# Performance work log

Measured on AMD Instinct MI355X. Metric: run time of the kernel, lower is better.

## Reference

```python
import jax, jax.numpy as jnp
import numpy as np

N_NODES = 50000
N_EDGES = 800000
GEN_EPS = 1e-7
LN_EPS = 1e-5


def _mlp3_tanh(x, w0, b0, w1, b1, w2, b2):
    x = jnp.tanh(x @ w0.T + b0)
    x = jnp.tanh(x @ w1.T + b1)
    return jnp.tanh(x @ w2.T + b2)


def _gen_conv(x, src, dst, edge_attr, w0, b0, ln_w, ln_b, w1, b1):
    # GENConv(aggr='softmax', t=1): msg = relu(x_j + e) + eps
    msg = jax.nn.relu(x[src] + edge_attr) + GEN_EPS          # [E, 64]
    m = jax.ops.segment_max(msg, dst, num_segments=N_NODES)  # [N, 64]
    ex = jnp.exp(msg - m[dst])
    den = jax.ops.segment_sum(ex, dst, num_segments=N_NODES)
    alpha = ex / den[dst]                                    # scatter-softmax per dst
    agg = jax.ops.segment_sum(alpha * msg, dst, num_segments=N_NODES)
    h = x + agg                                              # x_r + aggregated messages
    # internal MLP: Linear(64->128), LayerNorm(128), ReLU, Linear(128->64)
    h = h @ w0.T + b0
    mu = jnp.mean(h, axis=-1, keepdims=True)
    var = jnp.mean((h - mu) ** 2, axis=-1, keepdims=True)
    h = ln_w * (h - mu) * jax.lax.rsqrt(var + LN_EPS) + ln_b
    h = jax.nn.relu(h)
    return h @ w1.T + b1


def setup_inputs() -> dict:
    key = jax.random.key(0)
    ks = jax.random.split(key, 32)
    s = 0.05
    d = {
        'node_features': jax.random.normal(ks[0], (N_NODES, 11), jnp.float32),
        'edge_features': jax.random.normal(ks[1], (N_EDGES, 3), jnp.float32),
        'edge_index': jax.random.randint(ks[2], (2, N_EDGES), 0, N_NODES, jnp.int32),
        'ne_w0': jax.random.normal(ks[3], (64, 11)) * s, 'ne_b0': jnp.zeros((64,)),
        'ne_w1': jax.random.normal(ks[4], (64, 64)) * s, 'ne_b1': jnp.zeros((64,)),
        'ne_w2': jax.random.normal(ks[5], (64, 64)) * s, 'ne_b2': jnp.zeros((64,)),
        'ee_w0': jax.random.normal(ks[6], (64, 3)) * s, 'ee_b0': jnp.zeros((64,)),
        'ee_w1': jax.random.normal(ks[7], (64, 64)) * s, 'ee_b1': jnp.zeros((64,)),
        'ee_w2': jax.random.normal(ks[8], (64, 64)) * s, 'ee_b2': jnp.zeros((64,)),
        'mp_w0': jax.random.normal(ks[9], (3, 128, 64)) * s,
        'mp_b0': jnp.zeros((3, 128)),
        'mp_ln_w': jnp.ones((3, 128)), 'mp_ln_b': jnp.zeros((3, 128)),
        'mp_w1': jax.random.normal(ks[10], (3, 64, 128)) * s,
        'mp_b1': jnp.zeros((3, 64)),
        'pi_w0': jax.random.normal(ks[11], (64, 64)) * s, 'pi_b0': jnp.zeros((64,)),
        'pi_w1': jax.random.normal(ks[12], (64, 64)) * s, 'pi_b1': jnp.zeros((64,)),
        'pi_w2': jax.random.normal(ks[13], (2, 64)) * s, 'pi_b2': jnp.zeros((2,)),
    }
    return {k: (v.astype(jnp.float32) if v.dtype != jnp.int32 else v) for k, v in d.items()}


def reference(node_features, edge_features, edge_index,
              ne_w0, ne_b0, ne_w1, ne_b1, ne_w2, ne_b2,
              ee_w0, ee_b0, ee_w1, ee_b1, ee_w2, ee_b2,
              mp_w0, mp_b0, mp_ln_w, mp_ln_b, mp_w1, mp_b1,
              pi_w0, pi_b0, pi_w1, pi_b1, pi_w2, pi_b2):
    src, dst = edge_index[0], edge_index[1]
    x = _mlp3_tanh(node_features, ne_w0, ne_b0, ne_w1, ne_b1, ne_w2, ne_b2)
    e = _mlp3_tanh(edge_features, ee_w0, ee_b0, ee_w1, ee_b1, ee_w2, ee_b2)
    for i in range(3):
        x = _gen_conv(x, src, dst, e, mp_w0[i], mp_b0[i], mp_ln_w[i], mp_ln_b[i], mp_w1[i], mp_b1[i])
    h = jnp.tanh(x @ pi_w0.T + pi_b0)
    h = jnp.tanh(h @ pi_w1.T + pi_b1)
    out = h @ pi_w2.T + pi_b2                 # [N, 2]
    # output.t().reshape(-1)[:n_turbines] == first column of out
    means = -30.0 + (out[:, 0] + 1.0) * 60.0 / 2.0
    return means
```

## Files before the change

### kernel.cpp

```cpp
#include <hip/hip_runtime.h>
#include <hip/hip_fp16.h>
#include <stdint.h>

#define N_NODES 50000
#define N_EDGES 800000

typedef unsigned short u16;
typedef unsigned int u32;
typedef __attribute__((ext_vector_type(8))) short short8;
typedef __attribute__((ext_vector_type(4))) float f32x4;
typedef __attribute__((ext_vector_type(4))) u32 u32x4;
typedef __attribute__((ext_vector_type(2))) u32 u32x2;

#define WAVE_SYNC() asm volatile("s_waitcnt lgkmcnt(0)" ::: "memory")

__device__ __forceinline__ float b2f(u16 v) {
    u32 u = ((u32)v) << 16; float f; __builtin_memcpy(&f, &u, 4); return f;
}
__device__ __forceinline__ u16 f2b(float f) {
    u32 u; __builtin_memcpy(&u, &f, 4);
    return (u16)((u + 0x8000u) >> 16);
}
__device__ __forceinline__ float lo2f(u32 p) {
    u32 u = p << 16; float f; __builtin_memcpy(&f, &u, 4); return f;
}
__device__ __forceinline__ float hi2f(u32 p) {
    u32 u = p & 0xffff0000u; float f; __builtin_memcpy(&f, &u, 4); return f;
}
__device__ __forceinline__ u32 pack2(float a, float b) {
    u32 ua, ub; __builtin_memcpy(&ua, &a, 4); __builtin_memcpy(&ub, &b, 4);
    return __builtin_amdgcn_perm(ub + 0x8000u, ua + 0x8000u, 0x07060302u);
}
__device__ __forceinline__ f32x4 mfma16(short8 a, short8 b, f32x4 c) {
    return __builtin_amdgcn_mfma_f32_16x16x32_bf16(a, b, c, 0, 0, 0);
}

__device__ __forceinline__ bool detect_bf(const void* nf) {
    u32 w = ((const u32*)nf)[threadIdx.x & 63];
    u32 lo = w & 0xffffu;
    int e = (int)((lo >> 7) & 0xff);
    int good = ((e >= 118 && e <= 132) || lo == 0) ? 1 : 0;
    unsigned long long b = __ballot(good != 0);
    return __popcll(b) >= 48;
}

#define TANH_TBL_N 256
__device__ __forceinline__ void load_tbl(const u32* __restrict__ g, u32* tbl) {
    int i = (int)threadIdx.x;
    if (i < TANH_TBL_N) tbl[i] = g[i];
    __syncthreads();
}
__device__ __forceinline__ float lut_tanh(const u32* __restrict__ tbl, float x) {
    float a = __builtin_fabsf(x);
    a = fminf(a, 7.96875f);
    int i = (int)(a * 32.f);
    u32 e = tbl[i];
    __half2 h2; __builtin_memcpy(&h2, &e, 4);
    float b = __half2float(__low2half(h2));
    float s = __half2float(__high2half(h2));
    return copysignf(fmaf(s, a, b), x);
}

enum : int {
    NE_B0 = 704,   NE_B1 = 4864,  NE_B2 = 9024,
    EE_B0 = 9280,  EE_B1 = 13440, EE_B2 = 17600,
    MP_B0 = 42240, LNW_O = 42624, LNB_O = 43008, MP_B1 = 67968,
    PI_B0 = 72256, PI_B1 = 76416, PI_W2 = 76480, PI_B2 = 76608,
    W_TOTAL = 76610
};

enum : int {
    FR_EE1 = 0, FR_EE2 = 4, FR_EE3 = 12, FR_NE1 = 20, FR_NE2 = 24, FR_NE3 = 32,
    FR_MP0 = 40, FR_MP1 = 88, FR_PI0 = 136, FR_PI1 = 144, FR_TOTAL = 152
};

#define OFF_W       ((size_t)0)
#define OFF_WB      ((size_t)0x61000)
#define OFF_TBL     ((size_t)0x88000)
#define OFF_XB0     ((size_t)0x90000)
#define OFF_XB1     ((size_t)0x700000)
#define OFF_H64B    ((size_t)0xE00000)
#define OFF_E       ((size_t)0x1500000)
#define OFF_ROWPTR  ((size_t)0x8300000)
#define OFF_CURSOR  ((size_t)0x8340000)
#define OFF_CNT     ((size_t)0x8380000)
#define OFF_PERM    ((size_t)0x83C0000)
#define OFF_SRCS    ((size_t)0x8700000)
#define OFF_BSUM    ((size_t)0x8A80000)

struct Ptrs24 { const void* p[24]; };

__global__ void prep_kernel(const void* nf, Ptrs24 ps, float* __restrict__ W,
                            u16* __restrict__ Wb, u32* __restrict__ gtbl) {
    bool bf = detect_bf(nf);
    int t = blockIdx.x * blockDim.x + threadIdx.x;
    if (t < FR_TOTAL * 512) {
        const int base[15] = {FR_EE1,FR_EE2,FR_EE3,FR_NE1,FR_NE2,FR_NE3,
                              FR_MP0,FR_MP0+16,FR_MP0+32, FR_MP1,FR_MP1+16,FR_MP1+32,
                              FR_PI0,FR_PI1,FR_TOTAL};
        const int psrc[14]  = {6,8,10, 0,2,4, 12,12,12, 16,16,16, 18,20};
        const int soff[14]  = {0,0,0, 0,0,0, 0,8192,16384, 0,8192,16384, 0,0};
        const int kreal[14] = {3,64,64, 11,64,64, 64,64,64, 128,128,128, 64,64};
        const int nn[14]    = {64,64,64, 64,64,64, 128,128,128, 64,64,64, 64,64};
        int f = t >> 9, r = t & 511, lane = r >> 3, j = r & 7;
        int l = 0;
        while (f >= base[l + 1]) l++;
        int lf = f - base[l];
        int NT = nn[l] >> 4;
        int kt = lf / NT, nt = lf % NT;
        int k = kt * 32 + (lane >> 4) * 8 + j;
        int n = nt * 16 + (lane & 15);
        float v = 0.f;
        if (k < kreal[l]) {
            long idx = (long)soff[l] + (long)n * kreal[l] + k;
            const void* p = ps.p[psrc[l]];
            v = bf ? b2f(((const u16*)p)[idx]) : ((const float*)p)[idx];
        }
        u32 u; __builtin_memcpy(&u, &v, 4);
        Wb[t] = (u16)((u + 0x7fffu + ((u >> 16) & 1u)) >> 16);
        return;
    }
    int t2 = t - FR_TOTAL * 512;
    if (t2 < 1986) {
        const int cnt[14]  = {64,64,64, 64,64,64, 384,384,384,192, 64,64,128,2};
        const int wdst[14] = {NE_B0,NE_B1,NE_B2, EE_B0,EE_B1,EE_B2,
                              MP_B0,LNW_O,LNB_O,MP_B1, PI_B0,PI_B1,PI_W2,PI_B2};
        const int sp[14]   = {1,3,5, 7,9,11, 13,14,15,17, 19,21,22,23};
        int sgi = 0, off = t2;
        while (off >= cnt[sgi]) { off -= cnt[sgi]; sgi++; }
        const void* p = ps.p[sp[sgi]];
        W[wdst[sgi] + off] = bf ? b2f(((const u16*)p)[off]) : ((const float*)p)[off];
        return;
    }
    int i = t2 - 1986;
    if (i < TANH_TBL_N) {
        float x0 = i * 0.03125f, x1 = x0 + 0.03125f;
        float t0 = tanhf(x0), t1 = tanhf(x1);
        float s = (t1 - t0) * 32.f;
        float b = fmaf(-s, x0, t0);
        __half hs = __float2half(s), hb = __float2half(b);
        u16 us, ub;
        __builtin_memcpy(&us, &hs, 2); __builtin_memcpy(&ub, &hb, 2);
        gtbl[i] = (u32)ub | ((u32)us << 16);
    }
}


__global__ void hist_kernel(const int* __restrict__ dst, int* __restrict__ cnts) {
    int e = blockIdx.x * blockDim.x + threadIdx.x;
    if (e < N_EDGES) atomicAdd(&cnts[dst[e]], 1);
}

__global__ void scanA(const int* __restrict__ cnts, int* __restrict__ prow,
                      int* __restrict__ bsum) {
    __shared__ int wsum[16];
    int tid = threadIdx.x, lane = tid & 63, wid = tid >> 6;
    int i0 = blockIdx.x * 2048 + tid * 2;
    int v0 = 0, v1 = 0;
    if (i0 >= 1 && i0 <= N_NODES) v0 = (cnts[i0 - 1] + 1) & ~1;
    if (i0 + 1 <= N_NODES && i0 + 1 >= 1) v1 = (cnts[i0] + 1) & ~1;
    int v = v0 + v1;
#pragma unroll
    for (int off = 1; off < 64; off <<= 1) {
        int t = __shfl_up(v, off, 64);
        if (lane >= off) v += t;
    }
    if (lane == 63) wsum[wid] = v;
    __syncthreads();
    if (tid == 0) { int a = 0; for (int w = 0; w < 16; w++) { a += wsum[w]; wsum[w] = a; } }
    __syncthreads();
    int incl = v + (wid ? wsum[wid - 1] : 0);
    if (i0 <= N_NODES) prow[i0] = incl - v1;
    if (i0 + 1 <= N_NODES) prow[i0 + 1] = incl;
    if (tid == 1023) bsum[blockIdx.x] = incl;
}
__global__ void scanC(const int* __restrict__ bsum, const int* __restrict__ cnts,
                      int* __restrict__ prow, int* __restrict__ cursor,
                      int* __restrict__ srcs) {
    int i = blockIdx.x * 1024 + threadIdx.x;
    if (i > N_NODES) return;
    int nb = (int)(blockIdx.x >> 1);
    int add = 0;
    for (int b = 0; b < nb; b++) add += bsum[b];
    int v = prow[i] + add;
    prow[i] = v;
    if (i < N_NODES) {
        cursor[i] = v;
        int c = cnts[i];
        if (c & 1) srcs[v + c] = -1;
    }
}

__global__ void scatter_kernel(const int* __restrict__ dst, const int* __restrict__ src,
                               int* __restrict__ cursor, int* __restrict__ perm,
                               int* __restrict__ srcs) {
    int e = blockIdx.x * blockDim.x + threadIdx.x;
    if (e >= N_EDGES) return;
    int p = atomicAdd(&cursor[dst[e]], 1);
    perm[e] = p;
    srcs[p] = src[e];
}


template<int KT, int NT, int INSTR>
__device__ __forceinline__ void mfma_layer(const u32* ldsin, int lane,
        const short8* __restrict__ Wf, int basef, const float* __restrict__ bias, f32x4* acc) {
    int q = lane >> 4, mr = lane & 15;
#pragma unroll
    for (int nt = 0; nt < NT; nt++) acc[nt] = *(const f32x4*)(bias + nt * 16 + q * 4);
#pragma unroll
    for (int kt = 0; kt < KT; kt++) {
        short8 act = *(const short8*)(ldsin + mr * INSTR + kt * 16 + q * 4);
#pragma unroll
        for (int nt = 0; nt < NT; nt++)
            acc[nt] = mfma16(Wf[(basef + kt * NT + nt) * 64 + lane], act, acc[nt]);
    }
}

template<int KT, int NT>
__device__ __forceinline__ void mfma_layer_reg(const short8* act, int lane,
        const short8* __restrict__ Wf, int basef, const float* __restrict__ bias, f32x4* acc) {
    int q = lane >> 4;
#pragma unroll
    for (int nt = 0; nt < NT; nt++) acc[nt] = *(const f32x4*)(bias + nt * 16 + q * 4);
#pragma unroll
    for (int kt = 0; kt < KT; kt++)
#pragma unroll
        for (int nt = 0; nt < NT; nt++)
            acc[nt] = mfma16(Wf[(basef + kt * NT + nt) * 64 + lane], act[kt], acc[nt]);
}

template<int NT, int OUTSTR>
__device__ __forceinline__ void tanh_pack_lds(const f32x4* acc, u32* ldsout, int lane,
                                              const u32* __restrict__ tbl) {
    int q = lane >> 4, mr = lane & 15;
#pragma unroll
    for (int nt = 0; nt < NT; nt++) {
        f32x4 a = acc[nt];
        ldsout[mr * OUTSTR + nt * 8 + q * 2 + 0] = pack2(lut_tanh(tbl, a[0]), lut_tanh(tbl, a[1]));
        ldsout[mr * OUTSTR + nt * 8 + q * 2 + 1] = pack2(lut_tanh(tbl, a[2]), lut_tanh(tbl, a[3]));
    }
}

__device__ __forceinline__ void zero_stage(u32* B0, int lane) {
#pragma unroll
    for (int it = 0; it < 4; it++) {
        int f = lane + 64 * it;
        B0[(f >> 4) * 36 + (f & 15)] = 0;
    }
}


__global__ __launch_bounds__(256) void edge_encoder(const void* nf, const void* ef,
        u32* __restrict__ ebuf, const int* __restrict__ perm, const float* __restrict__ W,
        const short8* __restrict__ Wf, const u32* __restrict__ gtbl) {
    __shared__ u32 lds[4 * 1152];
    __shared__ u32 tbl[TANH_TBL_N];
    bool bf = detect_bf(nf);
    load_tbl(gtbl, tbl);
    int wv = threadIdx.x >> 6, lane = threadIdx.x & 63;
    u32* B0 = lds + wv * 1152;
    u32* B1 = B0 + 576;
    long ebase = (long)blockIdx.x * 64 + wv * 16;
    zero_stage(B0, lane);
    if (lane < 16) {
        long e = ebase + lane;
        float i0, i1, i2;
        if (bf) { const u16* p = (const u16*)ef + e * 3; i0 = b2f(p[0]); i1 = b2f(p[1]); i2 = b2f(p[2]); }
        else    { const float* p = (const float*)ef + e * 3; i0 = p[0]; i1 = p[1]; i2 = p[2]; }
        u32* row = B0 + lane * 36;
        row[0] = pack2(i0, i1); row[1] = pack2(i2, 0.f);
    }
    WAVE_SYNC();
    f32x4 acc[4];
    mfma_layer<1, 4, 36>(B0, lane, Wf, FR_EE1, W + EE_B0, acc);
    tanh_pack_lds<4, 36>(acc, B1, lane, tbl);
    WAVE_SYNC();
    mfma_layer<2, 4, 36>(B1, lane, Wf, FR_EE2, W + EE_B1, acc);
    tanh_pack_lds<4, 36>(acc, B0, lane, tbl);
    WAVE_SYNC();
    mfma_layer<2, 4, 36>(B0, lane, Wf, FR_EE3, W + EE_B2, acc);
    tanh_pack_lds<4, 36>(acc, B1, lane, tbl);
    WAVE_SYNC();
    int ro = lane >> 2, cc = (lane & 3) * 8;
    long e = ebase + ro;
    long prowp = perm[e];
    u32x4 v0 = *(const u32x4*)&B1[ro * 36 + cc];
    u32x4 v1 = *(const u32x4*)&B1[ro * 36 + cc + 4];
    *(u32x4*)&ebuf[prowp * 32 + cc] = v0;
    *(u32x4*)&ebuf[prowp * 32 + cc + 4] = v1;
}

__global__ __launch_bounds__(256) void node_encoder(const void* nf,
        u16* __restrict__ xbf, const float* __restrict__ W,
        const short8* __restrict__ Wf, const u32* __restrict__ gtbl) {
    __shared__ u32 lds[4 * 1152];
    __shared__ u32 tbl[TANH_TBL_N];
    bool bf = detect_bf(nf);
    load_tbl(gtbl, tbl);
    int wv = threadIdx.x >> 6, lane = threadIdx.x & 63;
    int q = lane >> 4, mr = lane & 15;
    u32* B0 = lds + wv * 1152;
    u32* B1 = B0 + 576;
    long nbase = (long)blockIdx.x * 64 + wv * 16;
    zero_stage(B0, lane);
    if (lane < 16) {
        long n = nbase + lane;
        if (n < N_NODES) {
            float in[11];
#pragma unroll
            for (int j = 0; j < 11; j++)
                in[j] = bf ? b2f(((const u16*)nf)[n * 11 + j]) : ((const float*)nf)[n * 11 + j];
            u32* row = B0 + lane * 36;
#pragma unroll
            for (int d = 0; d < 5; d++) row[d] = pack2(in[2 * d], in[2 * d + 1]);
            row[5] = pack2(in[10], 0.f);
        }
    }
    WAVE_SYNC();
    f32x4 acc[4];
    mfma_layer<1, 4, 36>(B0, lane, Wf, FR_NE1, W + NE_B0, acc);
    tanh_pack_lds<4, 36>(acc, B1, lane, tbl);
    WAVE_SYNC();
    mfma_layer<2, 4, 36>(B1, lane, Wf, FR_NE2, W + NE_B1, acc);
    tanh_pack_lds<4, 36>(acc, B0, lane, tbl);
    WAVE_SYNC();
    mfma_layer<2, 4, 36>(B0, lane, Wf, FR_NE3, W + NE_B2, acc);
    long n = nbase + mr;
    if (n < N_NODES) {
#pragma unroll
        for (int nt = 0; nt < 4; nt++) {
            float v0 = lut_tanh(tbl, acc[nt][0]), v1 = lut_tanh(tbl, acc[nt][1]);
            float v2 = lut_tanh(tbl, acc[nt][2]), v3 = lut_tanh(tbl, acc[nt][3]);
            u32x2 pb; pb.x = pack2(v0, v1); pb.y = pack2(v2, v3);
            *(u32x2*)&xbf[n * 64 + nt * 16 + q * 4] = pb;
        }
    }
}

template<int R>
__global__ __launch_bounds__(256) void aggregate_kernel(
        const u32* __restrict__ xbf32, const u32* __restrict__ ebuf32,
        const int* __restrict__ srcs, const int* __restrict__ prow,
        u32* __restrict__ h64bf32) {
    __shared__ int ldsW[4][64];
    int wv = threadIdx.x >> 6;
    int wid = (int)((blockIdx.x * 256 + threadIdx.x) >> 6);
    int lane = (int)(threadIdx.x & 63);
    int n0 = __builtin_amdgcn_readfirstlane(wid) * 2;
    if (n0 >= N_NODES) return;
    int half = lane >> 5, h = lane & 31;
    int rl = n0 + (lane < 2 ? lane : 2);
    int rv = prow[rl];
    int kb0 = __shfl(rv, 0, 64);
    int kb1 = __shfl(rv, 1, 64);
    int kb2 = __shfl(rv, 2, 64);
    float num[2][2], den[2][2];
#pragma unroll
    for (int j = 0; j < 2; j++) { num[j][0] = num[j][1] = den[j][0] = den[j][1] = 0.f; }
    for (int wb = kb0; wb < kb2; wb += 64) {
        ldsW[wv][lane] = srcs[wb + lane];
        WAVE_SYNC();
        int we = wb + 64;
        int hi0 = kb1 < we ? kb1 : we;
        int lo1 = kb1 > wb ? kb1 : wb;
        int hi1 = kb2 < we ? kb2 : we;
#pragma unroll 4
        for (int k = wb; k < hi0; k += 2) {
            int s = ldsW[wv][k - wb + half];
            u32 ev = ebuf32[(size_t)(k + half) * 32 + h];
            u32 xv = xbf32[(size_t)(s > 0 ? s : 0) * 32 + h];
            float m0 = fmaxf(lo2f(xv) + lo2f(ev), 0.f) + 1e-7f;
            float m1 = fmaxf(hi2f(xv) + hi2f(ev), 0.f) + 1e-7f;
            float w0 = __expf(m0), w1 = __expf(m1);
            if (s < 0) { w0 = 0.f; w1 = 0.f; }
            num[0][0] = fmaf(w0, m0, num[0][0]); den[0][0] += w0;
            num[0][1] = fmaf(w1, m1, num[0][1]); den[0][1] += w1;
        }
#pragma unroll 4
        for (int k = lo1; k < hi1; k += 2) {
            int s = ldsW[wv][k - wb + half];
            u32 ev = ebuf32[(size_t)(k + half) * 32 + h];
            u32 xv = xbf32[(size_t)(s > 0 ? s : 0) * 32 + h];
            float m0 = fmaxf(lo2f(xv) + lo2f(ev), 0.f) + 1e-7f;
            float m1 = fmaxf(hi2f(xv) + hi2f(ev), 0.f) + 1e-7f;
            float w0 = __expf(m0), w1 = __expf(m1);
            if (s < 0) { w0 = 0.f; w1 = 0.f; }
            num[1][0] = fmaf(w0, m0, num[1][0]); den[1][0] += w0;
            num[1][1] = fmaf(w1, m1, num[1][1]); den[1][1] += w1;
        }
        WAVE_SYNC();
    }
#pragma unroll
    for (int j = 0; j < 2; j++) {
        float n0f = num[j][0] + __shfl_xor(num[j][0], 32, 64);
        float d0f = den[j][0] + __shfl_xor(den[j][0], 32, 64);
        float n1f = num[j][1] + __shfl_xor(num[j][1], 32, 64);
        float d1f = den[j][1] + __shfl_xor(den[j][1], 32, 64);
        if (half == 0) {
            float agg0 = (d0f > 0.f) ? __fdividef(n0f, d0f) : 0.f;
            float agg1 = (d1f > 0.f) ? __fdividef(n1f, d1f) : 0.f;
            u32 xr = xbf32[(size_t)(n0 + j) * 32 + h];
            h64bf32[(size_t)(n0 + j) * 32 + h] = pack2(lo2f(xr) + agg0, hi2f(xr) + agg1);
        }
    }
}

__global__ __launch_bounds__(256) void mlp_fused(const u16* __restrict__ h64bf,
        u16* __restrict__ xbf,
        const float* __restrict__ W, const short8* __restrict__ Wf, int r) {
    __shared__ u32 lds[4 * 1088];
    int wv = threadIdx.x >> 6, lane = threadIdx.x & 63;
    int q = lane >> 4, mr = lane & 15;
    u32* bufY = lds + wv * 1088;
    long nbase = (long)blockIdx.x * 64 + wv * 16;
    long row = nbase + mr;
    long rc = (row < N_NODES) ? row : (N_NODES - 1);
    short8 act[2];
#pragma unroll
    for (int kt = 0; kt < 2; kt++)
        act[kt] = *(const short8*)&h64bf[rc * 64 + kt * 32 + q * 8];
    f32x4 acc[8];
    mfma_layer_reg<2, 8>(act, lane, Wf, FR_MP0 + r * 16, W + MP_B0 + r * 128, acc);
    float s = 0.f, sq = 0.f;
#pragma unroll
    for (int nt = 0; nt < 8; nt++)
#pragma unroll
        for (int rr = 0; rr < 4; rr++) { float v = acc[nt][rr]; s += v; sq = fmaf(v, v, sq); }
    s += __shfl_xor(s, 16, 64);  s += __shfl_xor(s, 32, 64);
    sq += __shfl_xor(sq, 16, 64); sq += __shfl_xor(sq, 32, 64);
    float mu = s * (1.f / 128.f);
    float var = sq * (1.f / 128.f) - mu * mu;
    float inv = rsqrtf(var + 1e-5f);
    const float* LW = W + LNW_O + r * 128;
    const float* LB = W + LNB_O + r * 128;
#pragma unroll
    for (int nt = 0; nt < 8; nt++) {
        f32x4 lw = *(const f32x4*)(LW + nt * 16 + q * 4);
        f32x4 lb = *(const f32x4*)(LB + nt * 16 + q * 4);
        float u0 = fmaxf(fmaf((acc[nt][0] - mu) * inv, lw[0], lb[0]), 0.f);
        float u1 = fmaxf(fmaf((acc[nt][1] - mu) * inv, lw[1], lb[1]), 0.f);
        float u2 = fmaxf(fmaf((acc[nt][2] - mu) * inv, lw[2], lb[2]), 0.f);
        float u3 = fmaxf(fmaf((acc[nt][3] - mu) * inv, lw[3], lb[3]), 0.f);
        bufY[mr * 68 + nt * 8 + q * 2 + 0] = pack2(u0, u1);
        bufY[mr * 68 + nt * 8 + q * 2 + 1] = pack2(u2, u3);
    }
    WAVE_SYNC();
    f32x4 acc2[4];
    mfma_layer<4, 4, 68>(bufY, lane, Wf, FR_MP1 + r * 16, W + MP_B1 + r * 64, acc2);
    if (row < N_NODES) {
#pragma unroll
        for (int nt = 0; nt < 4; nt++) {
            f32x4 v = acc2[nt];
            u32x2 pb; pb.x = pack2(v[0], v[1]); pb.y = pack2(v[2], v[3]);
            *(u32x2*)&xbf[row * 64 + nt * 16 + q * 4] = pb;
        }
    }
}

__global__ __launch_bounds__(256) void policy_head(const void* nf,
        const u16* __restrict__ xbf, void* out, const float* __restrict__ W,
        const short8* __restrict__ Wf, const u32* __restrict__ gtbl) {
    __shared__ u32 lds[4 * 576];
    __shared__ u32 tbl[TANH_TBL_N];
    bool bf = detect_bf(nf);
    load_tbl(gtbl, tbl);
    int wv = threadIdx.x >> 6, lane = threadIdx.x & 63;
    int q = lane >> 4, mr = lane & 15;
    u32* bufY = lds + wv * 576;
    long nbase = (long)blockIdx.x * 64 + wv * 16;
    long row = nbase + mr;
    long rc = (row < N_NODES) ? row : (N_NODES - 1);
    short8 act[2];
#pragma unroll
    for (int kt = 0; kt < 2; kt++)
        act[kt] = *(const short8*)&xbf[rc * 64 + kt * 32 + q * 8];
    f32x4 acc[4];
    mfma_layer_reg<2, 4>(act, lane, Wf, FR_PI0, W + PI_B0, acc);
    tanh_pack_lds<4, 36>(acc, bufY, lane, tbl);
    WAVE_SYNC();
    mfma_layer<2, 4, 36>(bufY, lane, Wf, FR_PI1, W + PI_B1, acc);
    float o = 0.f;
#pragma unroll
    for (int nt = 0; nt < 4; nt++) {
        f32x4 w2 = *(const f32x4*)(W + PI_W2 + nt * 16 + q * 4);
#pragma unroll
        for (int rr = 0; rr < 4; rr++) o = fmaf(lut_tanh(tbl, acc[nt][rr]), w2[rr], o);
    }
    o += __shfl_xor(o, 16, 64);
    o += __shfl_xor(o, 32, 64);
    if (lane < 16 && row < N_NODES) {
        float means = 30.f * (o + W[PI_B2]);
        if (bf) ((u16*)out)[row] = f2b(means);
        else    ((float*)out)[row] = means;
    }
}

extern "C" void kernel_launch(void* const* d_in, const int* in_sizes, int n_in,
                              void* d_out, int out_size, void* d_ws, size_t ws_size,
                              hipStream_t stream) {
    char* ws = (char*)d_ws;
    float* W      = (float*)(ws + OFF_W);
    u16*   Wb     = (u16*)(ws + OFF_WB);
    const short8* Wf = (const short8*)(ws + OFF_WB);
    u32*   gtbl   = (u32*)(ws + OFF_TBL);
    u16*   xb0    = (u16*)(ws + OFF_XB0);
    u16*   xb1    = (u16*)(ws + OFF_XB1);
    u16*   h64bf  = (u16*)(ws + OFF_H64B);
    u32*   h64b32 = (u32*)(ws + OFF_H64B);
    u32*   ebuf32 = (u32*)(ws + OFF_E);
    int*   prow   = (int*)(ws + OFF_ROWPTR);
    int*   cursor = (int*)(ws + OFF_CURSOR);
    int*   cnts   = (int*)(ws + OFF_CNT);
    int*   perm   = (int*)(ws + OFF_PERM);
    int*   srcs   = (int*)(ws + OFF_SRCS);
    int*   bsum   = (int*)(ws + OFF_BSUM);

    const void* nf  = d_in[0];
    const int* ei   = (const int*)d_in[2];
    const int* srcv = ei;
    const int* dstv = ei + N_EDGES;

    hipMemsetAsync(cnts, 0, N_NODES * sizeof(int), stream);

    Ptrs24 ps;
    for (int k = 0; k < 24; k++) ps.p[k] = d_in[3 + k];
    prep_kernel<<<(FR_TOTAL * 512 + 1986 + TANH_TBL_N + 255) / 256, 256, 0, stream>>>(
        nf, ps, W, Wb, gtbl);

    hist_kernel<<<(N_EDGES + 255) / 256, 256, 0, stream>>>(dstv, cnts);
    scanA<<<25, 1024, 0, stream>>>(cnts, prow, bsum);
    scanC<<<(N_NODES + 1024) / 1024, 1024, 0, stream>>>(bsum, cnts, prow, cursor, srcs);
    scatter_kernel<<<(N_EDGES + 255) / 256, 256, 0, stream>>>(dstv, srcv, cursor, perm, srcs);

    node_encoder<<<(N_NODES + 63) / 64, 256, 0, stream>>>(nf, xb0, W, Wf, gtbl);
    edge_encoder<<<N_EDGES / 64, 256, 0, stream>>>(nf, d_in[1], ebuf32, perm, W, Wf, gtbl);

    u16* xbc = xb0; u16* xbn = xb1;
    const int aggBlocks = (N_NODES / 2 * 64) / 256;
    aggregate_kernel<0><<<aggBlocks, 256, 0, stream>>>((const u32*)xbc, ebuf32, srcs, prow, h64b32);
    mlp_fused<<<(N_NODES + 63) / 64, 256, 0, stream>>>(h64bf, xbn, W, Wf, 0);
    { u16* tb = xbc; xbc = xbn; xbn = tb; }
    aggregate_kernel<1><<<aggBlocks, 256, 0, stream>>>((const u32*)xbc, ebuf32, srcs, prow, h64b32);
    mlp_fused<<<(N_NODES + 63) / 64, 256, 0, stream>>>(h64bf, xbn, W, Wf, 1);
    { u16* tb = xbc; xbc = xbn; xbn = tb; }
    aggregate_kernel<2><<<aggBlocks, 256, 0, stream>>>((const u32*)xbc, ebuf32, srcs, prow, h64b32);
    mlp_fused<<<(N_NODES + 63) / 64, 256, 0, stream>>>(h64bf, xbn, W, Wf, 2);
    { u16* tb = xbc; xbc = xbn; xbn = tb; }

    policy_head<<<(N_NODES + 63) / 64, 256, 0, stream>>>(nf, xbc, d_out, W, Wf, gtbl);
}
```

Before: 420.8 us.

## Fold count zeroing into prep, widen aggregation loads, write edge encodings directly

Zeroing of the histogram counts moves into prep_kernel, so the separate memset launch goes away. The edge encoder writes its final tanh output straight to the permuted global edge buffer instead of staging it through LDS. LDS stores in the tanh/LayerNorm paths are merged into 64-bit writes. The aggregation kernel now handles four edges per iteration, with each lane loading 8-byte pairs instead of 4-byte words. This raises memory-level parallelism but adds tail masking and uses smaller, 8-byte scattered global writes in the edge encoder.

```diff
diff --git a/kernel.cpp b/kernel.cpp
--- a/kernel.cpp
+++ b/kernel.cpp
@@ -90,11 +90,17 @@
 
 struct Ptrs24 { const void* p[24]; };
 
+#define PREP_FRAG   (FR_TOTAL * 512)
+#define PREP_BIAS   (PREP_FRAG + 1986)
+#define PREP_LUT    (PREP_BIAS + TANH_TBL_N)
+#define PREP_TOTAL  (PREP_LUT + N_NODES)
+
 __global__ void prep_kernel(const void* nf, Ptrs24 ps, float* __restrict__ W,
-                            u16* __restrict__ Wb, u32* __restrict__ gtbl) {
+                            u16* __restrict__ Wb, u32* __restrict__ gtbl,
+                            int* __restrict__ cnts) {
     bool bf = detect_bf(nf);
     int t = blockIdx.x * blockDim.x + threadIdx.x;
-    if (t < FR_TOTAL * 512) {
+    if (t < PREP_FRAG) {
         const int base[15] = {FR_EE1,FR_EE2,FR_EE3,FR_NE1,FR_NE2,FR_NE3,
                               FR_MP0,FR_MP0+16,FR_MP0+32, FR_MP1,FR_MP1+16,FR_MP1+32,
                               FR_PI0,FR_PI1,FR_TOTAL};
@@ -120,8 +126,8 @@
         Wb[t] = (u16)((u + 0x7fffu + ((u >> 16) & 1u)) >> 16);
         return;
     }
-    int t2 = t - FR_TOTAL * 512;
-    if (t2 < 1986) {
+    if (t < PREP_BIAS) {
+        int t2 = t - PREP_FRAG;
         const int cnt[14]  = {64,64,64, 64,64,64, 384,384,384,192, 64,64,128,2};
         const int wdst[14] = {NE_B0,NE_B1,NE_B2, EE_B0,EE_B1,EE_B2,
                               MP_B0,LNW_O,LNB_O,MP_B1, PI_B0,PI_B1,PI_W2,PI_B2};
@@ -132,8 +138,8 @@
         W[wdst[sgi] + off] = bf ? b2f(((const u16*)p)[off]) : ((const float*)p)[off];
         return;
     }
-    int i = t2 - 1986;
-    if (i < TANH_TBL_N) {
+    if (t < PREP_LUT) {
+        int i = t - PREP_BIAS;
         float x0 = i * 0.03125f, x1 = x0 + 0.03125f;
         float t0 = tanhf(x0), t1 = tanhf(x1);
         float s = (t1 - t0) * 32.f;
@@ -142,7 +148,9 @@
         u16 us, ub;
         __builtin_memcpy(&us, &hs, 2); __builtin_memcpy(&ub, &hb, 2);
         gtbl[i] = (u32)ub | ((u32)us << 16);
-    }
+        return;
+    }
+    if (t < PREP_TOTAL) cnts[t - PREP_LUT] = 0;
 }
 
 
@@ -237,8 +245,10 @@
 #pragma unroll
     for (int nt = 0; nt < NT; nt++) {
         f32x4 a = acc[nt];
-        ldsout[mr * OUTSTR + nt * 8 + q * 2 + 0] = pack2(lut_tanh(tbl, a[0]), lut_tanh(tbl, a[1]));
-        ldsout[mr * OUTSTR + nt * 8 + q * 2 + 1] = pack2(lut_tanh(tbl, a[2]), lut_tanh(tbl, a[3]));
+        u32x2 pb;
+        pb.x = pack2(lut_tanh(tbl, a[0]), lut_tanh(tbl, a[1]));
+        pb.y = pack2(lut_tanh(tbl, a[2]), lut_tanh(tbl, a[3]));
+        *(u32x2*)&ldsout[mr * OUTSTR + nt * 8 + q * 2] = pb;
     }
 }
 
@@ -259,6 +269,7 @@
     bool bf = detect_bf(nf);
     load_tbl(gtbl, tbl);
     int wv = threadIdx.x >> 6, lane = threadIdx.x & 63;
+    int q = lane >> 4, mr = lane & 15;
     u32* B0 = lds + wv * 1152;
     u32* B1 = B0 + 576;
     long ebase = (long)blockIdx.x * 64 + wv * 16;
@@ -280,15 +291,15 @@
     tanh_pack_lds<4, 36>(acc, B0, lane, tbl);
     WAVE_SYNC();
     mfma_layer<2, 4, 36>(B0, lane, Wf, FR_EE3, W + EE_B2, acc);
-    tanh_pack_lds<4, 36>(acc, B1, lane, tbl);
-    WAVE_SYNC();
-    int ro = lane >> 2, cc = (lane & 3) * 8;
-    long e = ebase + ro;
-    long prowp = perm[e];
-    u32x4 v0 = *(const u32x4*)&B1[ro * 36 + cc];
-    u32x4 v1 = *(const u32x4*)&B1[ro * 36 + cc + 4];
-    *(u32x4*)&ebuf[prowp * 32 + cc] = v0;
-    *(u32x4*)&ebuf[prowp * 32 + cc + 4] = v1;
+    int prw = perm[ebase + mr];
+    size_t gb = (size_t)prw * 32 + (size_t)(q * 2);
+#pragma unroll
+    for (int nt = 0; nt < 4; nt++) {
+        u32x2 pb;
+        pb.x = pack2(lut_tanh(tbl, acc[nt][0]), lut_tanh(tbl, acc[nt][1]));
+        pb.y = pack2(lut_tanh(tbl, acc[nt][2]), lut_tanh(tbl, acc[nt][3]));
+        *(u32x2*)&ebuf[gb + nt * 8] = pb;
+    }
 }
 
 __global__ __launch_bounds__(256) void node_encoder(const void* nf,
@@ -330,9 +341,9 @@
     if (n < N_NODES) {
 #pragma unroll
         for (int nt = 0; nt < 4; nt++) {
-            float v0 = lut_tanh(tbl, acc[nt][0]), v1 = lut_tanh(tbl, acc[nt][1]);
-            float v2 = lut_tanh(tbl, acc[nt][2]), v3 = lut_tanh(tbl, acc[nt][3]);
-            u32x2 pb; pb.x = pack2(v0, v1); pb.y = pack2(v2, v3);
+            u32x2 pb;
+            pb.x = pack2(lut_tanh(tbl, acc[nt][0]), lut_tanh(tbl, acc[nt][1]));
+            pb.y = pack2(lut_tanh(tbl, acc[nt][2]), lut_tanh(tbl, acc[nt][3]));
             *(u32x2*)&xbf[n * 64 + nt * 16 + q * 4] = pb;
         }
     }
@@ -349,15 +360,17 @@
     int lane = (int)(threadIdx.x & 63);
     int n0 = __builtin_amdgcn_readfirstlane(wid) * 2;
     if (n0 >= N_NODES) return;
-    int half = lane >> 5, h = lane & 31;
+    int qt = lane >> 4, h16 = lane & 15;
     int rl = n0 + (lane < 2 ? lane : 2);
     int rv = prow[rl];
     int kb0 = __shfl(rv, 0, 64);
     int kb1 = __shfl(rv, 1, 64);
     int kb2 = __shfl(rv, 2, 64);
-    float num[2][2], den[2][2];
-#pragma unroll
-    for (int j = 0; j < 2; j++) { num[j][0] = num[j][1] = den[j][0] = den[j][1] = 0.f; }
+    float an[2][4], ad[2][4];
+#pragma unroll
+    for (int j = 0; j < 2; j++)
+#pragma unroll
+        for (int f = 0; f < 4; f++) { an[j][f] = 0.f; ad[j][f] = 0.f; }
     for (int wb = kb0; wb < kb2; wb += 64) {
         ldsW[wv][lane] = srcs[wb + lane];
         WAVE_SYNC();
@@ -365,43 +378,65 @@
         int hi0 = kb1 < we ? kb1 : we;
         int lo1 = kb1 > wb ? kb1 : wb;
         int hi1 = kb2 < we ? kb2 : we;
-#pragma unroll 4
-        for (int k = wb; k < hi0; k += 2) {
-            int s = ldsW[wv][k - wb + half];
-            u32 ev = ebuf32[(size_t)(k + half) * 32 + h];
-            u32 xv = xbf32[(size_t)(s > 0 ? s : 0) * 32 + h];
-            float m0 = fmaxf(lo2f(xv) + lo2f(ev), 0.f) + 1e-7f;
-            float m1 = fmaxf(hi2f(xv) + hi2f(ev), 0.f) + 1e-7f;
-            float w0 = __expf(m0), w1 = __expf(m1);
-            if (s < 0) { w0 = 0.f; w1 = 0.f; }
-            num[0][0] = fmaf(w0, m0, num[0][0]); den[0][0] += w0;
-            num[0][1] = fmaf(w1, m1, num[0][1]); den[0][1] += w1;
-        }
-#pragma unroll 4
-        for (int k = lo1; k < hi1; k += 2) {
-            int s = ldsW[wv][k - wb + half];
-            u32 ev = ebuf32[(size_t)(k + half) * 32 + h];
-            u32 xv = xbf32[(size_t)(s > 0 ? s : 0) * 32 + h];
-            float m0 = fmaxf(lo2f(xv) + lo2f(ev), 0.f) + 1e-7f;
-            float m1 = fmaxf(hi2f(xv) + hi2f(ev), 0.f) + 1e-7f;
-            float w0 = __expf(m0), w1 = __expf(m1);
-            if (s < 0) { w0 = 0.f; w1 = 0.f; }
-            num[1][0] = fmaf(w0, m0, num[1][0]); den[1][0] += w0;
-            num[1][1] = fmaf(w1, m1, num[1][1]); den[1][1] += w1;
+#pragma unroll 2
+        for (int k = wb; k < hi0; k += 4) {
+            int e = k + qt;
+            int eoc = (e < hi0) ? e : (hi0 - 1);
+            int s = ldsW[wv][eoc - wb];
+            u32x2 ev = *(const u32x2*)&ebuf32[(size_t)eoc * 32 + 2 * h16];
+            u32x2 xv = *(const u32x2*)&xbf32[(size_t)(s > 0 ? s : 0) * 32 + 2 * h16];
+            float vf = (e < hi0 && s >= 0) ? 1.f : 0.f;
+            float m0 = fmaxf(lo2f(xv.x) + lo2f(ev.x), 0.f) + 1e-7f;
+            float m1 = fmaxf(hi2f(xv.x) + hi2f(ev.x), 0.f) + 1e-7f;
+            float m2 = fmaxf(lo2f(xv.y) + lo2f(ev.y), 0.f) + 1e-7f;
+            float m3 = fmaxf(hi2f(xv.y) + hi2f(ev.y), 0.f) + 1e-7f;
+            float w0 = __expf(m0) * vf, w1 = __expf(m1) * vf;
+            float w2 = __expf(m2) * vf, w3 = __expf(m3) * vf;
+            an[0][0] = fmaf(w0, m0, an[0][0]); ad[0][0] += w0;
+            an[0][1] = fmaf(w1, m1, an[0][1]); ad[0][1] += w1;
+            an[0][2] = fmaf(w2, m2, an[0][2]); ad[0][2] += w2;
+            an[0][3] = fmaf(w3, m3, an[0][3]); ad[0][3] += w3;
+        }
+#pragma unroll 2
+        for (int k = lo1; k < hi1; k += 4) {
+            int e = k + qt;
+            int eoc = (e < hi1) ? e : (hi1 - 1);
+            int s = ldsW[wv][eoc - wb];
+            u32x2 ev = *(const u32x2*)&ebuf32[(size_t)eoc * 32 + 2 * h16];
+            u32x2 xv = *(const u32x2*)&xbf32[(size_t)(s > 0 ? s : 0) * 32 + 2 * h16];
+            float vf = (e < hi1 && s >= 0) ? 1.f : 0.f;
+            float m0 = fmaxf(lo2f(xv.x) + lo2f(ev.x), 0.f) + 1e-7f;
+            float m1 = fmaxf(hi2f(xv.x) + hi2f(ev.x), 0.f) + 1e-7f;
+            float m2 = fmaxf(lo2f(xv.y) + lo2f(ev.y), 0.f) + 1e-7f;
+            float m3 = fmaxf(hi2f(xv.y) + hi2f(ev.y), 0.f) + 1e-7f;
+            float w0 = __expf(m0) * vf, w1 = __expf(m1) * vf;
+            float w2 = __expf(m2) * vf, w3 = __expf(m3) * vf;
+            an[1][0] = fmaf(w0, m0, an[1][0]); ad[1][0] += w0;
+            an[1][1] = fmaf(w1, m1, an[1][1]); ad[1][1] += w1;
+            an[1][2] = fmaf(w2, m2, an[1][2]); ad[1][2] += w2;
+            an[1][3] = fmaf(w3, m3, an[1][3]); ad[1][3] += w3;
         }
         WAVE_SYNC();
     }
 #pragma unroll
     for (int j = 0; j < 2; j++) {
-        float n0f = num[j][0] + __shfl_xor(num[j][0], 32, 64);
-        float d0f = den[j][0] + __shfl_xor(den[j][0], 32, 64);
-        float n1f = num[j][1] + __shfl_xor(num[j][1], 32, 64);
-        float d1f = den[j][1] + __shfl_xor(den[j][1], 32, 64);
-        if (half == 0) {
-            float agg0 = (d0f > 0.f) ? __fdividef(n0f, d0f) : 0.f;
-            float agg1 = (d1f > 0.f) ? __fdividef(n1f, d1f) : 0.f;
-            u32 xr = xbf32[(size_t)(n0 + j) * 32 + h];
-            h64bf32[(size_t)(n0 + j) * 32 + h] = pack2(lo2f(xr) + agg0, hi2f(xr) + agg1);
+#pragma unroll
+        for (int f = 0; f < 4; f++) {
+            an[j][f] += __shfl_xor(an[j][f], 16, 64);
+            an[j][f] += __shfl_xor(an[j][f], 32, 64);
+            ad[j][f] += __shfl_xor(ad[j][f], 16, 64);
+            ad[j][f] += __shfl_xor(ad[j][f], 32, 64);
+        }
+        if (qt == 0) {
+            float a0 = (ad[j][0] > 0.f) ? __fdividef(an[j][0], ad[j][0]) : 0.f;
+            float a1 = (ad[j][1] > 0.f) ? __fdividef(an[j][1], ad[j][1]) : 0.f;
+            float a2 = (ad[j][2] > 0.f) ? __fdividef(an[j][2], ad[j][2]) : 0.f;
+            float a3 = (ad[j][3] > 0.f) ? __fdividef(an[j][3], ad[j][3]) : 0.f;
+            u32x2 xr = *(const u32x2*)&xbf32[(size_t)(n0 + j) * 32 + 2 * h16];
+            u32x2 o;
+            o.x = pack2(lo2f(xr.x) + a0, hi2f(xr.x) + a1);
+            o.y = pack2(lo2f(xr.y) + a2, hi2f(xr.y) + a3);
+            *(u32x2*)&h64bf32[(size_t)(n0 + j) * 32 + 2 * h16] = o;
         }
     }
 }
@@ -442,8 +477,8 @@
         float u1 = fmaxf(fmaf((acc[nt][1] - mu) * inv, lw[1], lb[1]), 0.f);
         float u2 = fmaxf(fmaf((acc[nt][2] - mu) * inv, lw[2], lb[2]), 0.f);
         float u3 = fmaxf(fmaf((acc[nt][3] - mu) * inv, lw[3], lb[3]), 0.f);
-        bufY[mr * 68 + nt * 8 + q * 2 + 0] = pack2(u0, u1);
-        bufY[mr * 68 + nt * 8 + q * 2 + 1] = pack2(u2, u3);
+        u32x2 pb; pb.x = pack2(u0, u1); pb.y = pack2(u2, u3);
+        *(u32x2*)&bufY[mr * 68 + nt * 8 + q * 2] = pb;
     }
     WAVE_SYNC();
     f32x4 acc2[4];
@@ -521,12 +556,9 @@
     const int* srcv = ei;
     const int* dstv = ei + N_EDGES;
 
-    hipMemsetAsync(cnts, 0, N_NODES * sizeof(int), stream);
-
     Ptrs24 ps;
     for (int k = 0; k < 24; k++) ps.p[k] = d_in[3 + k];
-    prep_kernel<<<(FR_TOTAL * 512 + 1986 + TANH_TBL_N + 255) / 256, 256, 0, stream>>>(
-        nf, ps, W, Wb, gtbl);
+    prep_kernel<<<(PREP_TOTAL + 255) / 256, 256, 0, stream>>>(nf, ps, W, Wb, gtbl, cnts);
 
     hist_kernel<<<(N_EDGES + 255) / 256, 256, 0, stream>>>(dstv, cnts);
     scanA<<<25, 1024, 0, stream>>>(cnts, prow, bsum);
```

After: 439.4 us. 4.4% more time.
